# Optimization experiments

Hardware: AMD Instinct MI355X
Metric: run time of the kernel (lower is better)

## Reference

```python
import jax, jax.numpy as jnp
import numpy as np

N_NODES = 500_000
N_EDGES = 5_000_000
D = 16


def setup_inputs() -> dict:
    key = jax.random.key(0)
    k1, k2, k3, k4 = jax.random.split(key, 4)
    x = jax.random.normal(k1, (N_NODES, D), dtype=jnp.float32)
    edge_index = jax.random.randint(k2, (2, N_EDGES), 0, N_NODES, dtype=jnp.int32)
    # SAGEConv params: lin_l (applied to aggregated neighbors, carries bias),
    # lin_r (applied to root/self features, no bias). Torch Linear stores W as [out, in].
    scale = 1.0 / np.sqrt(D)
    W_l = jax.random.uniform(k3, (D, D), minval=-scale, maxval=scale, dtype=jnp.float32)
    b_l = jnp.zeros((D,), dtype=jnp.float32)
    W_r = jax.random.uniform(k4, (D, D), minval=-scale, maxval=scale, dtype=jnp.float32)
    return {"x": x, "edge_index": edge_index, "W_l": W_l, "b_l": b_l, "W_r": W_r}


def reference(x, edge_index, W_l, b_l, W_r):
    src = edge_index[0]  # message sources (x_j)
    dst = edge_index[1]  # aggregation targets (i)
    n = x.shape[0]
    # mean aggregation of neighbor features per destination node
    agg = jax.ops.segment_sum(x[src], dst, num_segments=n)  # [N, D]
    cnt = jax.ops.segment_sum(jnp.ones((src.shape[0],), dtype=x.dtype), dst, num_segments=n)
    mean = agg / jnp.maximum(cnt, 1.0)[:, None]
    # out = lin_l(mean) + lin_r(x)
    return mean @ W_l.T + b_l + x @ W_r.T
```

## Files before the change

### kernel.cpp

```cpp
#include <hip/hip_runtime.h>

#define N_NODES 500000
#define N_EDGES 5000000
#define D 16
#define BSH 9
#define BSZ 512
#define NB ((N_NODES + BSZ - 1) / BSZ)
#define CH 16384
#define PBLK ((N_EDGES + CH - 1) / CH)

__global__ __launch_bounds__(256) void hist_k(const int* __restrict__ edst,
                                              int* __restrict__ bhist) {
    __shared__ int h[NB];
    for (int i = threadIdx.x; i < NB; i += 256) h[i] = 0;
    __syncthreads();
    int stride = gridDim.x * blockDim.x;
    for (int e = blockIdx.x * blockDim.x + threadIdx.x; e < N_EDGES; e += stride)
        atomicAdd(&h[edst[e] >> BSH], 1);
    __syncthreads();
    for (int i = threadIdx.x; i < NB; i += 256)
        if (h[i]) atomicAdd(&bhist[i], h[i]);
}

__global__ void scan_k(const int* __restrict__ bhist, int* __restrict__ boff,
                       int* __restrict__ cursor) {
    __shared__ int s[1024];
    int t = threadIdx.x;
    int v = (t < NB) ? bhist[t] : 0;
    s[t] = v; __syncthreads();
    for (int off = 1; off < 1024; off <<= 1) {
        int u = (t >= off) ? s[t - off] : 0;
        __syncthreads(); s[t] += u; __syncthreads();
    }
    if (t < NB) { int ex = s[t] - v; boff[t] = ex; cursor[t] = ex; }
    if (t == 0) boff[NB] = N_EDGES;
}

__global__ __launch_bounds__(256) void place_k(const int* __restrict__ esrc,
                                               const int* __restrict__ edst,
                                               int* __restrict__ cursor,
                                               unsigned* __restrict__ rec) {
    __shared__ int lc[NB];
    int t = threadIdx.x;
    for (int i = t; i < NB; i += 256) lc[i] = 0;
    __syncthreads();
    int e0 = blockIdx.x * CH;
    int e1 = e0 + CH; if (e1 > N_EDGES) e1 = N_EDGES;
    for (int e = e0 + t; e < e1; e += 256)
        atomicAdd(&lc[edst[e] >> BSH], 1);
    __syncthreads();
    for (int i = t; i < NB; i += 256) {
        int c = lc[i];
        if (c) lc[i] = atomicAdd(&cursor[i], c);
    }
    __syncthreads();
    for (int e = e0 + t; e < e1; e += 256) {
        int dd = edst[e];
        int b = dd >> BSH;
        int p = atomicAdd(&lc[b], 1);
        rec[p] = ((unsigned)(dd & (BSZ - 1)) << 19) | (unsigned)esrc[e];
    }
}

__global__ __launch_bounds__(512, 8) void reduce_k(
    const float* __restrict__ x, const unsigned* __restrict__ rec,
    const int* __restrict__ boff, const float* __restrict__ Wl,
    const float* __restrict__ bl, const float* __restrict__ Wr,
    float* __restrict__ out) {
    __shared__ float slice[BSZ * D];
    __shared__ int scnt[BSZ];
    __shared__ unsigned srec[1024];
    int t = threadIdx.x;
    for (int i = t; i < BSZ * D; i += 512) slice[i] = 0.f;
    for (int i = t; i < BSZ; i += 512) scnt[i] = 0;

    int d = t & 15, g = t >> 4;
    int b = blockIdx.x;
    int beg = boff[b], end = boff[b + 1];

    for (int c0 = beg; c0 < end; c0 += 1024) {
        int cn = end - c0; if (cn > 1024) cn = 1024;
        __syncthreads();
        for (int i = t; i < cn; i += 512) srec[i] = rec[c0 + i];
        __syncthreads();

        int nfull = cn >> 8;
        for (int bb = 0; bb < nfull; ++bb) {
            int base = bb * 256 + g * 8;
            unsigned rc[8];
#pragma unroll
            for (int j = 0; j < 8; ++j) rc[j] = srec[base + j];
            float v[8];
#pragma unroll
            for (int j = 0; j < 8; ++j)
                v[j] = x[(int)(rc[j] & 0x7FFFFu) * D + d];
#pragma unroll
            for (int j = 0; j < 8; ++j) {
                int nl = (int)(rc[j] >> 19);
                atomicAdd(&slice[nl * D + d], v[j]);
                if (d == 0) atomicAdd(&scnt[nl], 1);
            }
        }
        for (int i = (nfull << 8) + g; i < cn; i += 32) {
            unsigned rc = srec[i];
            int src = (int)(rc & 0x7FFFFu);
            int nl  = (int)(rc >> 19);
            atomicAdd(&slice[nl * D + d], x[src * D + d]);
            if (d == 0) atomicAdd(&scnt[nl], 1);
        }
    }
    __syncthreads();

    float wl[D], wr[D];
    const float4* wl4 = (const float4*)(Wl + d * D);
    const float4* wr4 = (const float4*)(Wr + d * D);
#pragma unroll
    for (int q = 0; q < 4; ++q) {
        float4 a = wl4[q], b2 = wr4[q];
        wl[4*q]=a.x; wl[4*q+1]=a.y; wl[4*q+2]=a.z; wl[4*q+3]=a.w;
        wr[4*q]=b2.x; wr[4*q+1]=b2.y; wr[4*q+2]=b2.z; wr[4*q+3]=b2.w;
    }
    float bb = bl[d];
    int node0 = b << BSH;
    for (int n = g; n < BSZ; n += 32) {
        int node = node0 + n;
        if (node >= N_NODES) break;
        float m  = slice[n * D + d] / fmaxf((float)scnt[n], 1.f);
        float xv = x[node * D + d];
        float o  = bb;
#pragma unroll
        for (int k = 0; k < D; ++k)
            o += __shfl(m, k, 16) * wl[k] + __shfl(xv, k, 16) * wr[k];
        out[node * D + d] = o;
    }
}

__global__ void sage_scatter(const float* __restrict__ x, const int* __restrict__ esrc,
                             const int* __restrict__ edst, float* __restrict__ agg,
                             float* __restrict__ cnt) {
    long long gid = (long long)blockIdx.x * blockDim.x + threadIdx.x;
    long long e = gid >> 4;
    int d = (int)(gid & 15);
    if (e >= N_EDGES) return;
    atomicAdd(&agg[(long long)edst[e] * D + d], x[(long long)esrc[e] * D + d]);
    if (d == 0) atomicAdd(&cnt[edst[e]], 1.0f);
}

__global__ void sage_finalize(const float* __restrict__ x, float* __restrict__ agg_out,
                              const float* __restrict__ cnt, const float* __restrict__ W_l,
                              const float* __restrict__ b_l, const float* __restrict__ W_r) {
    __shared__ float sWl[D * D], sWr[D * D], sb[D];
    int tid = threadIdx.x;
    if (tid < D * D) { sWl[tid] = W_l[tid]; sWr[tid] = W_r[tid]; }
    if (tid < D) sb[tid] = b_l[tid];
    __syncthreads();
    int i = blockIdx.x * blockDim.x + tid;
    if (i >= N_NODES) return;
    float inv = 1.0f / fmaxf(cnt[i], 1.0f);
    float m[D], xv[D];
    const float4* ap = (const float4*)(agg_out + (long long)i * D);
    const float4* xp = (const float4*)(x + (long long)i * D);
#pragma unroll
    for (int q = 0; q < 4; ++q) {
        float4 a = ap[q], b = xp[q];
        m[4*q]=a.x*inv; m[4*q+1]=a.y*inv; m[4*q+2]=a.z*inv; m[4*q+3]=a.w*inv;
        xv[4*q]=b.x; xv[4*q+1]=b.y; xv[4*q+2]=b.z; xv[4*q+3]=b.w;
    }
    float o[D];
#pragma unroll
    for (int oo = 0; oo < D; ++oo) {
        float a2 = sb[oo];
#pragma unroll
        for (int k = 0; k < D; ++k) a2 += m[k]*sWl[oo*D+k] + xv[k]*sWr[oo*D+k];
        o[oo] = a2;
    }
    float4* op = (float4*)(agg_out + (long long)i * D);
#pragma unroll
    for (int q = 0; q < 4; ++q)
        op[q] = make_float4(o[4*q], o[4*q+1], o[4*q+2], o[4*q+3]);
}

extern "C" void kernel_launch(void* const* d_in, const int* in_sizes, int n_in,
                              void* d_out, int out_size, void* d_ws, size_t ws_size,
                              hipStream_t stream) {
    const float* x   = (const float*)d_in[0];
    const int*   ei  = (const int*)d_in[1];
    const float* W_l = (const float*)d_in[2];
    const float* b_l = (const float*)d_in[3];
    const float* W_r = (const float*)d_in[4];
    const int* esrc = ei;
    const int* edst = ei + N_EDGES;
    float* out = (float*)d_out;

    size_t rec_b = (size_t)N_EDGES * 4;
    size_t need  = rec_b + (size_t)(3 * NB + 1) * 4;

    if (ws_size >= need) {
        unsigned* rec = (unsigned*)d_ws;
        int* bhist  = (int*)((char*)d_ws + rec_b);
        int* boff   = bhist + NB;
        int* cursor = boff + (NB + 1);

        hipMemsetAsync(bhist, 0, (size_t)NB * 4, stream);
        hist_k<<<512, 256, 0, stream>>>(edst, bhist);
        scan_k<<<1, 1024, 0, stream>>>(bhist, boff, cursor);
        place_k<<<PBLK, 256, 0, stream>>>(esrc, edst, cursor, rec);
        reduce_k<<<NB, 512, 0, stream>>>(x, rec, boff, W_l, b_l, W_r, out);
    } else {
        float* cntf = (float*)d_ws;
        hipMemsetAsync(out, 0, (size_t)N_NODES * D * sizeof(float), stream);
        hipMemsetAsync(cntf, 0, (size_t)N_NODES * sizeof(float), stream);
        long long total = (long long)N_EDGES * D;
        sage_scatter<<<(unsigned)((total + 255) / 256), 256, 0, stream>>>(x, esrc, edst, out, cntf);
        sage_finalize<<<(N_NODES + 255) / 256, 256, 0, stream>>>(x, out, cntf, W_l, b_l, W_r);
    }
}
```

Before: 594.3 us.

## Sub-bucket edges by source range to improve gather locality in reduce

Edges are now bucketed by destination block and by one of eight source-index ranges, so records inside each destination bucket are grouped by source region. The histogram, scan and placement kernels work on the larger key space, and the scan handles eight bins per thread. The aim is better cache locality for the x gathers in the reduce kernel. The cost is more shared-memory histogram bins (about 7.8K ints, around 31 KB) in the hist and place kernels, which can lower their occupancy, plus a wider scan.

```diff
diff --git a/kernel.cpp b/kernel.cpp
--- a/kernel.cpp
+++ b/kernel.cpp
@@ -6,65 +6,83 @@
 #define BSH 9
 #define BSZ 512
 #define NB ((N_NODES + BSZ - 1) / BSZ)
+#define TSH 16
+#define NT 8
+#define NBK (NB * NT)
 #define CH 16384
 #define PBLK ((N_EDGES + CH - 1) / CH)
 
-__global__ __launch_bounds__(256) void hist_k(const int* __restrict__ edst,
+__global__ __launch_bounds__(256) void hist_k(const int* __restrict__ esrc,
+                                              const int* __restrict__ edst,
                                               int* __restrict__ bhist) {
-    __shared__ int h[NB];
-    for (int i = threadIdx.x; i < NB; i += 256) h[i] = 0;
+    __shared__ int h[NBK];
+    for (int i = threadIdx.x; i < NBK; i += 256) h[i] = 0;
     __syncthreads();
     int stride = gridDim.x * blockDim.x;
-    for (int e = blockIdx.x * blockDim.x + threadIdx.x; e < N_EDGES; e += stride)
-        atomicAdd(&h[edst[e] >> BSH], 1);
-    __syncthreads();
-    for (int i = threadIdx.x; i < NB; i += 256)
+    for (int e = blockIdx.x * blockDim.x + threadIdx.x; e < N_EDGES; e += stride) {
+        int key = ((edst[e] >> BSH) << 3) | (esrc[e] >> TSH);
+        atomicAdd(&h[key], 1);
+    }
+    __syncthreads();
+    for (int i = threadIdx.x; i < NBK; i += 256)
         if (h[i]) atomicAdd(&bhist[i], h[i]);
 }
 
-__global__ void scan_k(const int* __restrict__ bhist, int* __restrict__ boff,
+__global__ void scan_k(const int* __restrict__ bhist, int* __restrict__ boffk,
                        int* __restrict__ cursor) {
     __shared__ int s[1024];
     int t = threadIdx.x;
-    int v = (t < NB) ? bhist[t] : 0;
-    s[t] = v; __syncthreads();
+    int v[8]; int sum = 0;
+#pragma unroll
+    for (int j = 0; j < 8; ++j) {
+        int i = 8 * t + j;
+        v[j] = (i < NBK) ? bhist[i] : 0;
+        sum += v[j];
+    }
+    s[t] = sum; __syncthreads();
     for (int off = 1; off < 1024; off <<= 1) {
         int u = (t >= off) ? s[t - off] : 0;
         __syncthreads(); s[t] += u; __syncthreads();
     }
-    if (t < NB) { int ex = s[t] - v; boff[t] = ex; cursor[t] = ex; }
-    if (t == 0) boff[NB] = N_EDGES;
+    int base = s[t] - sum;
+#pragma unroll
+    for (int j = 0; j < 8; ++j) {
+        int i = 8 * t + j;
+        if (i < NBK) { boffk[i] = base; cursor[i] = base; }
+        base += v[j];
+    }
+    if (t == 1023) boffk[NBK] = N_EDGES;
 }
 
 __global__ __launch_bounds__(256) void place_k(const int* __restrict__ esrc,
                                                const int* __restrict__ edst,
                                                int* __restrict__ cursor,
                                                unsigned* __restrict__ rec) {
-    __shared__ int lc[NB];
+    __shared__ int lc[NBK];
     int t = threadIdx.x;
-    for (int i = t; i < NB; i += 256) lc[i] = 0;
+    for (int i = t; i < NBK; i += 256) lc[i] = 0;
     __syncthreads();
     int e0 = blockIdx.x * CH;
     int e1 = e0 + CH; if (e1 > N_EDGES) e1 = N_EDGES;
     for (int e = e0 + t; e < e1; e += 256)
-        atomicAdd(&lc[edst[e] >> BSH], 1);
-    __syncthreads();
-    for (int i = t; i < NB; i += 256) {
+        atomicAdd(&lc[((edst[e] >> BSH) << 3) | (esrc[e] >> TSH)], 1);
+    __syncthreads();
+    for (int i = t; i < NBK; i += 256) {
         int c = lc[i];
         if (c) lc[i] = atomicAdd(&cursor[i], c);
     }
     __syncthreads();
     for (int e = e0 + t; e < e1; e += 256) {
-        int dd = edst[e];
-        int b = dd >> BSH;
-        int p = atomicAdd(&lc[b], 1);
-        rec[p] = ((unsigned)(dd & (BSZ - 1)) << 19) | (unsigned)esrc[e];
+        int dd = edst[e], ss = esrc[e];
+        int key = ((dd >> BSH) << 3) | (ss >> TSH);
+        int p = atomicAdd(&lc[key], 1);
+        rec[p] = ((unsigned)(dd & (BSZ - 1)) << 19) | (unsigned)ss;
     }
 }
 
 __global__ __launch_bounds__(512, 8) void reduce_k(
     const float* __restrict__ x, const unsigned* __restrict__ rec,
-    const int* __restrict__ boff, const float* __restrict__ Wl,
+    const int* __restrict__ boffk, const float* __restrict__ Wl,
     const float* __restrict__ bl, const float* __restrict__ Wr,
     float* __restrict__ out) {
     __shared__ float slice[BSZ * D];
@@ -76,7 +94,7 @@
 
     int d = t & 15, g = t >> 4;
     int b = blockIdx.x;
-    int beg = boff[b], end = boff[b + 1];
+    int beg = boffk[b << 3], end = boffk[(b + 1) << 3];
 
     for (int c0 = beg; c0 < end; c0 += 1024) {
         int cn = end - c0; if (cn > 1024) cn = 1024;
@@ -103,10 +121,8 @@
         }
         for (int i = (nfull << 8) + g; i < cn; i += 32) {
             unsigned rc = srec[i];
-            int src = (int)(rc & 0x7FFFFu);
-            int nl  = (int)(rc >> 19);
-            atomicAdd(&slice[nl * D + d], x[src * D + d]);
-            if (d == 0) atomicAdd(&scnt[nl], 1);
+            atomicAdd(&slice[(int)(rc >> 19) * D + d], x[(int)(rc & 0x7FFFFu) * D + d]);
+            if (d == 0) atomicAdd(&scnt[rc >> 19], 1);
         }
     }
     __syncthreads();
@@ -120,14 +136,14 @@
         wl[4*q]=a.x; wl[4*q+1]=a.y; wl[4*q+2]=a.z; wl[4*q+3]=a.w;
         wr[4*q]=b2.x; wr[4*q+1]=b2.y; wr[4*q+2]=b2.z; wr[4*q+3]=b2.w;
     }
-    float bb = bl[d];
+    float bb2 = bl[d];
     int node0 = b << BSH;
     for (int n = g; n < BSZ; n += 32) {
         int node = node0 + n;
         if (node >= N_NODES) break;
         float m  = slice[n * D + d] / fmaxf((float)scnt[n], 1.f);
         float xv = x[node * D + d];
-        float o  = bb;
+        float o  = bb2;
 #pragma unroll
         for (int k = 0; k < D; ++k)
             o += __shfl(m, k, 16) * wl[k] + __shfl(xv, k, 16) * wr[k];
@@ -193,19 +209,19 @@
     float* out = (float*)d_out;
 
     size_t rec_b = (size_t)N_EDGES * 4;
-    size_t need  = rec_b + (size_t)(3 * NB + 1) * 4;
+    size_t need  = rec_b + (size_t)(3 * NBK + 1) * 4;
 
     if (ws_size >= need) {
         unsigned* rec = (unsigned*)d_ws;
         int* bhist  = (int*)((char*)d_ws + rec_b);
-        int* boff   = bhist + NB;
-        int* cursor = boff + (NB + 1);
-
-        hipMemsetAsync(bhist, 0, (size_t)NB * 4, stream);
-        hist_k<<<512, 256, 0, stream>>>(edst, bhist);
-        scan_k<<<1, 1024, 0, stream>>>(bhist, boff, cursor);
+        int* boffk  = bhist + NBK;
+        int* cursor = boffk + (NBK + 1);
+
+        hipMemsetAsync(bhist, 0, (size_t)NBK * 4, stream);
+        hist_k<<<512, 256, 0, stream>>>(esrc, edst, bhist);
+        scan_k<<<1, 1024, 0, stream>>>(bhist, boffk, cursor);
         place_k<<<PBLK, 256, 0, stream>>>(esrc, edst, cursor, rec);
-        reduce_k<<<NB, 512, 0, stream>>>(x, rec, boff, W_l, b_l, W_r, out);
+        reduce_k<<<NB, 512, 0, stream>>>(x, rec, boffk, W_l, b_l, W_r, out);
     } else {
         float* cntf = (float*)d_ws;
         hipMemsetAsync(out, 0, (size_t)N_NODES * D * sizeof(float), stream);
```

New measurement: 636.3 us. +7.1%, slower.
